# Kernel tuning notes

Measured on AMD Instinct MI355X. Metric: run time of the kernel, lower is better.

The kernel has to match this reference:

```python
import jax, jax.numpy as jnp
import numpy as np

POOLING_COUNTS = [15, 8, 8, 8]
N = 128


def _build_entries():
    """Replicates SparseMaxPool.__init__: per step (kernel, pool_stride, i_idx, j_idx)."""
    entries = []
    stride, offset = 1, 0
    for ci, c in enumerate(POOLING_COUNTS):
        for k in range(c):
            offset += stride
            # pooler layout: first block all MaxPool1d(2,1); later blocks start with MaxPool1d(3,2)
            kernel = 3 if (ci > 0 and k == 0) else 2
            pstride = 2 if kernel == 3 else 1
            i = np.arange(0, N - offset, stride)
            j = np.arange(offset, N, stride)
            entries.append((kernel, pstride, i, j))
        stride *= 2
    return entries

_ENTRIES = _build_entries()


def _maxpool1d(x, kernel, stride):
    # x: [B, D, L] -> [B, D, (L-kernel)//stride + 1]
    L = x.shape[-1]
    out = (L - kernel) // stride + 1
    slices = [x[..., t : t + (out - 1) * stride + 1 : stride] for t in range(kernel)]
    y = slices[0]
    for s in slices[1:]:
        y = jnp.maximum(y, s)
    return y


def setup_inputs() -> dict:
    key = jax.random.key(0)
    x = jax.random.normal(key, (16, 256, N), dtype=jnp.float32)
    return {"x": x}


def reference(x):
    B, D, Nv = x.shape
    map2d = jnp.zeros((B, D, N, N), dtype=x.dtype)
    diag = np.arange(N)
    map2d = map2d.at[:, :, diag, diag].set(x)
    for kernel, pstride, i, j in _ENTRIES:
        x = _maxpool1d(x, kernel, pstride)
        map2d = map2d.at[:, :, i, j].set(x)
    return map2d
```

## Files before the change

kernel.cpp:

```cpp
#include <hip/hip_runtime.h>


#define NN 128
#define SLICE_ELEMS (NN * NN)

__device__ __forceinline__ float entry_val(const float* __restrict__ buf, int r, int c) {
    int o = c - r;
    int w = o + 1;
    int wcl = w < 1 ? 1 : w;
    int k = 31 - __clz(wcl);
    int p2 = 1 << k;
    int lb = 129 * k - (p2 - 1);
    int d2 = wcl - p2;
    int oc = o < 1 ? 1 : o;
    int t = 31 - __clz(oc);
    int sh = t - 3;
    sh = sh < 0 ? 0 : (sh > 3 ? 3 : sh);
    int m = (1 << sh) - 1;
    bool valid = (o >= 0) & ((o & m) == m) & ((r & m) == 0);
    float v = fmaxf(buf[lb + r], buf[lb + r + d2]);
    return valid ? v : 0.0f;
}

__global__ __launch_bounds__(256) void sparse_maxpool_kernel(
        const float* __restrict__ x, float* __restrict__ out) {
    __shared__ float buf[1040];
    const int tid = threadIdx.x;
    const int slice = blockIdx.x;

    if (tid < NN) buf[tid] = x[(size_t)slice * NN + tid];
    __syncthreads();

    int base_prev = 0, base_cur = NN;
    #pragma unroll
    for (int k = 1; k <= 7; ++k) {
        int half = 1 << (k - 1);
        int len = (NN + 1) - (1 << k);
        if (tid < len)
            buf[base_cur + tid] = fmaxf(buf[base_prev + tid], buf[base_prev + tid + half]);
        __syncthreads();
        base_prev = base_cur;
        base_cur += len;
    }

    float4* __restrict__ out_s = reinterpret_cast<float4*>(out + (size_t)slice * SLICE_ELEMS);
    #pragma unroll
    for (int it = 0; it < 16; ++it) {
        int idx = it * 256 + tid;
        int r = idx >> 5;
        int c0 = (idx & 31) << 2;
        float4 v;
        v.x = entry_val(buf, r, c0);
        v.y = entry_val(buf, r, c0 + 1);
        v.z = entry_val(buf, r, c0 + 2);
        v.w = entry_val(buf, r, c0 + 3);
        out_s[idx] = v;
    }
}

extern "C" void kernel_launch(void* const* d_in, const int* in_sizes, int n_in,
                              void* d_out, int out_size, void* d_ws, size_t ws_size,
                              hipStream_t stream) {
    const float* x = (const float*)d_in[0];
    float* out = (float*)d_out;
    const int slices = in_sizes[0] / NN;
    sparse_maxpool_kernel<<<dim3(slices), dim3(256), 0, stream>>>(x, out);
}
```

Measured before the change: 258.3 us.

## Precompute gather descriptor tables and materialize valid values in LDS

A new init kernel builds two index tables in workspace: per-output-element LDS addresses (pointing at a zero slot for invalid positions) and per-valid-value source pairs. The main kernel first computes the 2560 distinct valid values into LDS, then fills each output float4 with pure table-driven LDS gathers, replacing per-element clz/mask arithmetic. This trades ALU work for an extra kernel launch plus global descriptor reads, though the kernel is likely bound by its 128 MB of output writes.

```diff
diff --git a/kernel.cpp b/kernel.cpp
--- a/kernel.cpp
+++ b/kernel.cpp
@@ -3,32 +3,75 @@
 
 #define NN 128
 #define SLICE_ELEMS (NN * NN)
+#define VOFF 784
+#define NVAL 2560
+#define ZERO_SLOT (VOFF + NVAL)
+#define LDS_WORDS (VOFF + NVAL + 1)
+#define NBUILD 2560
+#define NODESC 16384
 
-__device__ __forceinline__ float entry_val(const float* __restrict__ buf, int r, int c) {
-    int o = c - r;
-    int w = o + 1;
-    int wcl = w < 1 ? 1 : w;
-    int k = 31 - __clz(wcl);
-    int p2 = 1 << k;
-    int lb = 129 * k - (p2 - 1);
-    int d2 = wcl - p2;
-    int oc = o < 1 ? 1 : o;
-    int t = 31 - __clz(oc);
-    int sh = t - 3;
-    sh = sh < 0 ? 0 : (sh > 3 ? 3 : sh);
-    int m = (1 << sh) - 1;
-    bool valid = (o >= 0) & ((o & m) == m) & ((r & m) == 0);
-    float v = fmaxf(buf[lb + r], buf[lb + r + d2]);
-    return valid ? v : 0.0f;
+__device__ __forceinline__ void seg_params(int s, int& o, int& sh) {
+    if (s < 16)      { o = s;                sh = 0; }
+    else if (s < 24) { o = 17 + 2 * (s - 16); sh = 1; }
+    else if (s < 32) { o = 35 + 4 * (s - 24); sh = 2; }
+    else             { o = 71 + 8 * (s - 32); sh = 3; }
 }
 
-__global__ __launch_bounds__(256) void sparse_maxpool_kernel(
-        const float* __restrict__ x, float* __restrict__ out) {
-    __shared__ float buf[1040];
+__global__ __launch_bounds__(256) void sp_init(unsigned int* __restrict__ bdesc,
+                                               unsigned short* __restrict__ odesc) {
+    int idx = blockIdx.x * 256 + threadIdx.x;
+    if (idx < NODESC) {
+        int r = idx >> 7, c = idx & 127;
+        int o = c - r;
+        int sh = -1, s = 0;
+        if (o >= 0 && o <= 15)                          { sh = 0; s = o; }
+        else if (o >= 17 && o <= 31 && (o & 1) == 1)    { sh = 1; s = 16 + ((o - 17) >> 1); }
+        else if (o >= 35 && o <= 63 && (o & 3) == 3)    { sh = 2; s = 24 + ((o - 35) >> 2); }
+        else if (o >= 71 && o <= 127 && (o & 7) == 7)   { sh = 3; s = 32 + ((o - 71) >> 3); }
+        unsigned short addr = (unsigned short)ZERO_SLOT;
+        if (sh >= 0 && (r & ((1 << sh) - 1)) == 0) {
+            int base = 0;
+            for (int t = 0; t < s; ++t) {
+                int oo, ss; seg_params(t, oo, ss);
+                base += ((127 - oo) >> ss) + 1;
+            }
+            addr = (unsigned short)(VOFF + base + (r >> sh));
+        }
+        odesc[idx] = addr;
+    } else if (idx < NODESC + NBUILD) {
+        int i = idx - NODESC;
+        unsigned int desc = 0;
+        int base = 0;
+        for (int t = 0; t < 40; ++t) {
+            int oo, ss; seg_params(t, oo, ss);
+            int cnt = ((127 - oo) >> ss) + 1;
+            if (i < base + cnt) {
+                int r = (i - base) << ss;
+                int w = oo + 1;
+                int k = 31 - __clz(w);
+                int p2 = 1 << k;
+                int lb = 129 * k - (p2 - 1);
+                int s1 = lb + r;
+                int s2 = lb + r + (w - p2);
+                desc = (unsigned)s1 | ((unsigned)s2 << 16);
+                break;
+            }
+            base += cnt;
+        }
+        bdesc[i] = desc;
+    }
+}
+
+__global__ __launch_bounds__(256) void sp_main(const float* __restrict__ x,
+                                               float* __restrict__ out,
+                                               const unsigned int* __restrict__ bdesc,
+                                               const unsigned short* __restrict__ odesc) {
+    __shared__ float buf[LDS_WORDS];
     const int tid = threadIdx.x;
     const int slice = blockIdx.x;
 
     if (tid < NN) buf[tid] = x[(size_t)slice * NN + tid];
+    if (tid == 255) buf[ZERO_SLOT] = 0.0f;
     __syncthreads();
 
     int base_prev = 0, base_cur = NN;
@@ -43,17 +86,25 @@
         base_cur += len;
     }
 
+    #pragma unroll
+    for (int it = 0; it < NBUILD / 256; ++it) {
+        int i = it * 256 + tid;
+        unsigned int d = bdesc[i];
+        buf[VOFF + i] = fmaxf(buf[d & 0xffff], buf[d >> 16]);
+    }
+    __syncthreads();
+
     float4* __restrict__ out_s = reinterpret_cast<float4*>(out + (size_t)slice * SLICE_ELEMS);
+    const uint2* __restrict__ od = reinterpret_cast<const uint2*>(odesc);
     #pragma unroll
     for (int it = 0; it < 16; ++it) {
         int idx = it * 256 + tid;
-        int r = idx >> 5;
-        int c0 = (idx & 31) << 2;
+        uint2 d = od[idx];
         float4 v;
-        v.x = entry_val(buf, r, c0);
-        v.y = entry_val(buf, r, c0 + 1);
-        v.z = entry_val(buf, r, c0 + 2);
-        v.w = entry_val(buf, r, c0 + 3);
+        v.x = buf[d.x & 0xffff];
+        v.y = buf[d.x >> 16];
+        v.z = buf[d.y & 0xffff];
+        v.w = buf[d.y >> 16];
         out_s[idx] = v;
     }
 }
@@ -63,6 +114,12 @@
                               hipStream_t stream) {
     const float* x = (const float*)d_in[0];
     float* out = (float*)d_out;
+    unsigned int* bdesc = (unsigned int*)d_ws;
+    unsigned short* odesc = (unsigned short*)((char*)d_ws + NBUILD * 4);
+
+    const int init_items = NODESC + NBUILD;
+    sp_init<<<dim3((init_items + 255) / 256), dim3(256), 0, stream>>>(bdesc, odesc);
+
     const int slices = in_sizes[0] / NN;
-    sparse_maxpool_kernel<<<dim3(slices), dim3(256), 0, stream>>>(x, out);
+    sp_main<<<dim3(slices), dim3(256), 0, stream>>>(x, out, bdesc, odesc);
 }
```

After: 260.2 us. About the same (+0.7%).
